# Kernel tuning notes

Measured on AMD Instinct MI355X. Metric: run time of the kernel, lower is better.

The kernel has to match this reference:

```python
import jax, jax.numpy as jnp
import numpy as np

B, N, K = 8, 4096, 20          # 8 point clouds, 4096 points each, k=20 neighbors
C_IN, C_OUT = 64, 128
LN_EPS = 1e-5


def _layernorm(h, g, b):
    mu = jnp.mean(h, axis=-1, keepdims=True)
    var = jnp.var(h, axis=-1, keepdims=True)
    return (h - mu) * jax.lax.rsqrt(var + LN_EPS) * g + b


def setup_inputs() -> dict:
    key = jax.random.key(0)
    ks = jax.random.split(key, 8)
    x = jax.random.normal(ks[0], (B * N, C_IN), dtype=jnp.float32)
    batch = jnp.repeat(jnp.arange(B, dtype=jnp.int64), N)  # equal-size graphs
    def lin(k, fan_in, fan_out):
        bound = 1.0 / np.sqrt(fan_in)
        kw, kb = jax.random.split(k)
        W = jax.random.uniform(kw, (fan_in, fan_out), jnp.float32, -bound, bound)
        b = jax.random.uniform(kb, (fan_out,), jnp.float32, -bound, bound)
        return W, b
    W1, b1 = lin(ks[1], 2 * C_IN, C_OUT)
    W2, b2 = lin(ks[2], C_OUT, C_OUT)
    Wres, bres = lin(ks[3], C_IN, C_OUT)
    g1 = jnp.ones((C_OUT,), jnp.float32); be1 = jnp.zeros((C_OUT,), jnp.float32)
    g2 = jnp.ones((C_OUT,), jnp.float32); be2 = jnp.zeros((C_OUT,), jnp.float32)
    return dict(x=x, batch=batch, W1=W1, b1=b1, g1=g1, be1=be1,
                W2=W2, b2=b2, g2=g2, be2=be2, Wres=Wres, bres=bres)


def reference(x, batch, W1, b1, g1, be1, W2, b2, g2, be2, Wres, bres):
    # batch is contiguous equal-size segments -> reshape to [B, N, C]
    xb = x.reshape(B, N, C_IN)
    # KNN in feature space per cloud (DynamicEdgeConv semantics)
    sq = jnp.sum(xb * xb, axis=-1)                                 # [B, N]
    d2 = sq[:, :, None] + sq[:, None, :] - 2.0 * jnp.einsum('bnc,bmc->bnm', xb, xb)
    _, idx = jax.lax.top_k(-d2, K)                                  # [B, N, K], includes self
    # gather neighbor features
    xj = jnp.take_along_axis(xb[:, None, :, :].repeat(1, axis=1),
                             idx[..., None], axis=2) if False else \
         jax.vmap(lambda pts, ids: pts[ids])(xb, idx)               # [B, N, K, C_IN]
    xi = jnp.broadcast_to(xb[:, :, None, :], xj.shape)
    e = jnp.concatenate([xi, xj - xi], axis=-1)                     # [B, N, K, 2*C_IN]
    h = jax.nn.relu(_layernorm(jnp.einsum('bnkc,cd->bnkd', e, W1) + b1, g1, be1))
    h = jax.nn.relu(_layernorm(jnp.einsum('bnkd,de->bnke', h, W2) + b2, g2, be2))
    agg = jnp.max(h, axis=2)                                        # max aggregation over k
    out = agg.reshape(B * N, C_OUT) + (x @ Wres + bres)             # residual projection
    return out
```

## Files before the change

kernel.cpp:

```cpp
#include <hip/hip_runtime.h>
#include <hip/hip_bf16.h>


#define NB 8
#define NPTS 4096
#define KNN 20
#define NTOT (NB * NPTS)
#define NEDGE (NTOT * KNN)
#define LDA 136

typedef short bf16x8 __attribute__((ext_vector_type(8)));
typedef float f32x4 __attribute__((ext_vector_type(4)));

__device__ __forceinline__ unsigned short f2bf(float f) {
    union { float f; unsigned u; } v; v.f = f;
    unsigned r = v.u + 0x7FFFu + ((v.u >> 16) & 1u);
    return (unsigned short)(r >> 16);
}
__device__ __forceinline__ float bf2f(unsigned short s) {
    union { unsigned u; float f; } v; v.u = ((unsigned)s) << 16;
    return v.f;
}

__global__ __launch_bounds__(256) void k_prep(const float* __restrict__ x,
                                              unsigned short* __restrict__ xhi,
                                              unsigned short* __restrict__ xlo,
                                              float* __restrict__ sqn) {
    int id = blockIdx.x * 2048 + threadIdx.x * 8;
    float4 v0 = *(const float4*)(x + id);
    float4 v1 = *(const float4*)(x + id + 4);
    float vs[8] = {v0.x, v0.y, v0.z, v0.w, v1.x, v1.y, v1.z, v1.w};
    unsigned short h[8], l[8];
    float s = 0.f;
#pragma unroll
    for (int i = 0; i < 8; ++i) {
        h[i] = f2bf(vs[i]);
        l[i] = f2bf(vs[i] - bf2f(h[i]));
        s += vs[i] * vs[i];
    }
    uint4 hp, lp;
    hp.x = h[0] | ((unsigned)h[1] << 16); hp.y = h[2] | ((unsigned)h[3] << 16);
    hp.z = h[4] | ((unsigned)h[5] << 16); hp.w = h[6] | ((unsigned)h[7] << 16);
    lp.x = l[0] | ((unsigned)l[1] << 16); lp.y = l[2] | ((unsigned)l[3] << 16);
    lp.z = l[4] | ((unsigned)l[5] << 16); lp.w = l[6] | ((unsigned)l[7] << 16);
    *(uint4*)(xhi + id) = hp;
    *(uint4*)(xlo + id) = lp;
    s += __shfl_xor(s, 1); s += __shfl_xor(s, 2); s += __shfl_xor(s, 4);
    if ((threadIdx.x & 7) == 0) sqn[id >> 6] = -0.5f * s;
}

__global__ __launch_bounds__(256) void k_wt(const float* __restrict__ W1, const float* __restrict__ W2,
                                            const float* __restrict__ Wres,
                                            unsigned short* __restrict__ wa, unsigned short* __restrict__ wb,
                                            unsigned short* __restrict__ wrt, unsigned short* __restrict__ w2p) {
    int id = blockIdx.x * 256 + threadIdx.x;
    if (id < 16384) {
        int f = id >> 9, pos = id & 511;
        int lane = pos >> 3, m = pos & 7;
        int ks = f >> 3, nt = f & 7;
        int lr = lane & 15, kg = lane >> 4;
        int c = ks * 32 + kg * 8 + m;
        int d = nt * 16 + lr;
        w2p[id] = f2bf(W2[c * 128 + d]);
    } else if (id < 24576) {
        int i = id - 16384;
        int d = i >> 6, c = i & 63;
        wa[i] = f2bf(W1[c * 128 + d] - W1[(64 + c) * 128 + d]);
    } else if (id < 32768) {
        int i = id - 24576;
        int d = i >> 6, c = i & 63;
        wb[i] = f2bf(W1[(64 + c) * 128 + d]);
    } else {
        int i = id - 32768;
        int d = i >> 6, c = i & 63;
        wrt[i] = f2bf(Wres[c * 128 + d]);
    }
}

__global__ __launch_bounds__(512, 4) void k_knn(const float* __restrict__ x,
                                                const unsigned short* __restrict__ xhi,
                                                const unsigned short* __restrict__ xlo,
                                                const float* __restrict__ sqn,
                                                int* __restrict__ knn_idx) {
    int b  = blockIdx.x & 7;
    int qb = blockIdx.x >> 3;
    int t  = threadIdx.x;
    int w = t >> 6, lane = t & 63;
    int lr = lane & 15, kg = lane >> 4;
    int qgrp = w >> 1, tp = w & 1;
    int n0  = b * NPTS + qb * 64;
    int cb0 = b * NPTS;

    __shared__ union {
        unsigned short ring[2][2][8][512];
        struct { float md[64][161]; int ci[64][24]; } m;
        struct { float ce[64][24]; } r;
    } U;

    int qg = n0 + qgrp * 16 + lr;
    bf16x8 qhi0 = *(const bf16x8*)(xhi + (size_t)qg * 64 + kg * 8);
    bf16x8 qhi1 = *(const bf16x8*)(xhi + (size_t)qg * 64 + 32 + kg * 8);
    bf16x8 qlo0 = *(const bf16x8*)(xlo + (size_t)qg * 64 + kg * 8);
    bf16x8 qlo1 = *(const bf16x8*)(xlo + (size_t)qg * 64 + 32 + kg * 8);

    const unsigned short* splane = ((w >> 1) & 1) ? xlo : xhi;
    int stt = w >> 2, skh = w & 1;
    size_t soff = (size_t)(stt * 16 + (lane & 15)) * 64 + skh * 32 + (lane >> 4) * 8;

    float kd[KNN];
#pragma unroll
    for (int p = 0; p < KNN; ++p) kd[p] = 3.4e38f;
    int myq = qgrp * 16 + lr;

    {
        uint4 p0 = *(const uint4*)(splane + (size_t)cb0 * 64 + soff);
        uint4 p1 = *(const uint4*)(splane + (size_t)(cb0 + 32) * 64 + soff);
        *(uint4*)&U.ring[0][0][w][lane * 8] = p0;
        *(uint4*)&U.ring[0][1][w][lane * 8] = p1;
    }
    uint4 g0 = *(const uint4*)(splane + (size_t)(cb0 + 64) * 64 + soff);
    uint4 g1 = *(const uint4*)(splane + (size_t)(cb0 + 96) * 64 + soff);
    float4 sqc0 = *(const float4*)&sqn[cb0 + tp * 32 + kg * 4];
    float4 sqc1 = *(const float4*)&sqn[cb0 + tp * 32 + 16 + kg * 4];
    __syncthreads();

#pragma unroll 1
    for (int s = 0; s < 64; ++s) {
        if (s + 1 < 64) {
            *(uint4*)&U.ring[(s + 1) & 1][0][w][lane * 8] = g0;
            *(uint4*)&U.ring[(s + 1) & 1][1][w][lane * 8] = g1;
        }
        if (s + 2 < 64) {
            g0 = *(const uint4*)(splane + (size_t)(cb0 + (2 * s + 4) * 32) * 64 + soff);
            g1 = *(const uint4*)(splane + (size_t)(cb0 + (2 * s + 5) * 32) * 64 + soff);
        }
        float4 nsq0, nsq1;
        if (s + 1 < 64) {
            nsq0 = *(const float4*)&sqn[cb0 + (2 * (s + 1) + tp) * 32 + kg * 4];
            nsq1 = *(const float4*)&sqn[cb0 + (2 * (s + 1) + tp) * 32 + 16 + kg * 4];
        }

        const unsigned short* fr = &U.ring[s & 1][tp][0][0];
        bf16x8 A0 = *(const bf16x8*)(fr + 0 * 512 + lane * 8);
        bf16x8 A1 = *(const bf16x8*)(fr + 1 * 512 + lane * 8);
        bf16x8 A2 = *(const bf16x8*)(fr + 2 * 512 + lane * 8);
        bf16x8 A3 = *(const bf16x8*)(fr + 3 * 512 + lane * 8);
        bf16x8 A4 = *(const bf16x8*)(fr + 4 * 512 + lane * 8);
        bf16x8 A5 = *(const bf16x8*)(fr + 5 * 512 + lane * 8);
        bf16x8 A6 = *(const bf16x8*)(fr + 6 * 512 + lane * 8);
        bf16x8 A7 = *(const bf16x8*)(fr + 7 * 512 + lane * 8);

        f32x4 a00 = {sqc0.x, sqc0.y, sqc0.z, sqc0.w};
        f32x4 a01 = {0.f, 0.f, 0.f, 0.f};
        f32x4 a10 = {sqc1.x, sqc1.y, sqc1.z, sqc1.w};
        f32x4 a11 = {0.f, 0.f, 0.f, 0.f};
        a00 = __builtin_amdgcn_mfma_f32_16x16x32_bf16(A0, qhi0, a00, 0, 0, 0);
        a10 = __builtin_amdgcn_mfma_f32_16x16x32_bf16(A4, qhi0, a10, 0, 0, 0);
        a01 = __builtin_amdgcn_mfma_f32_16x16x32_bf16(A1, qhi1, a01, 0, 0, 0);
        a11 = __builtin_amdgcn_mfma_f32_16x16x32_bf16(A5, qhi1, a11, 0, 0, 0);
        a00 = __builtin_amdgcn_mfma_f32_16x16x32_bf16(A2, qhi0, a00, 0, 0, 0);
        a10 = __builtin_amdgcn_mfma_f32_16x16x32_bf16(A6, qhi0, a10, 0, 0, 0);
        a01 = __builtin_amdgcn_mfma_f32_16x16x32_bf16(A3, qhi1, a01, 0, 0, 0);
        a11 = __builtin_amdgcn_mfma_f32_16x16x32_bf16(A7, qhi1, a11, 0, 0, 0);
        a00 = __builtin_amdgcn_mfma_f32_16x16x32_bf16(A0, qlo0, a00, 0, 0, 0);
        a10 = __builtin_amdgcn_mfma_f32_16x16x32_bf16(A4, qlo0, a10, 0, 0, 0);
        a01 = __builtin_amdgcn_mfma_f32_16x16x32_bf16(A1, qlo1, a01, 0, 0, 0);
        a11 = __builtin_amdgcn_mfma_f32_16x16x32_bf16(A5, qlo1, a11, 0, 0, 0);

        int ibase = (2 * s + tp) * 32 + kg * 4;
#pragma unroll
        for (int j = 0; j < 8; ++j) {
            float sc = (j < 4) ? -(a00[j & 3] + a01[j & 3]) : -(a10[j & 3] + a11[j & 3]);
            unsigned idx12 = (unsigned)(ibase + ((j >> 2) << 4) + (j & 3));
            float xv = __uint_as_float((__float_as_uint(sc) & 0xFFFFF000u) | idx12);
#pragma unroll
            for (int p = KNN - 1; p >= 1; --p)
                kd[p] = __builtin_amdgcn_fmed3f(xv, kd[p - 1], kd[p]);
            kd[0] = fminf(kd[0], xv);
        }

        __syncthreads();
        sqc0 = nsq0; sqc1 = nsq1;
    }

    __syncthreads();
#pragma unroll
    for (int p = 0; p < KNN; ++p) U.m.md[myq][(tp * 4 + kg) * KNN + p] = kd[p];
    __syncthreads();

    if (t < 64) {
        float kdm[24];
#pragma unroll
        for (int s2 = 0; s2 < 24; ++s2) kdm[s2] = 3.4e38f;
        float km = 3.4e38f;
#pragma unroll 1
        for (int u = 0; u < 8; ++u) {
#pragma unroll 1
            for (int p = 0; p < KNN; ++p) {
                float d = U.m.md[t][u * KNN + p];
                if (d >= km) break;
#pragma unroll
                for (int s2 = 23; s2 >= 1; --s2)
                    kdm[s2] = __builtin_amdgcn_fmed3f(d, kdm[s2 - 1], kdm[s2]);
                kdm[0] = fminf(kdm[0], d);
                km = kdm[23];
            }
        }
#pragma unroll
        for (int s2 = 0; s2 < 24; ++s2)
            U.m.ci[t][s2] = (int)(__float_as_uint(kdm[s2]) & 0xFFFu) + cb0;
    }
    __syncthreads();

#pragma unroll 1
    for (int task = t; task < 1536; task += 512) {
        int q = task / 24, sl = task - q * 24;
        int cidx = U.m.ci[q][sl];
        const float* xqp = x + (size_t)(n0 + q) * 64;
        const float* xc  = x + (size_t)cidx * 64;
        float dot = 0.f;
#pragma unroll
        for (int g = 0; g < 16; ++g) {
            float4 a = *(const float4*)(xqp + g * 4);
            float4 bb = *(const float4*)(xc + g * 4);
            dot += a.x * bb.x + a.y * bb.y + a.z * bb.z + a.w * bb.w;
        }
        U.r.ce[q][sl] = -sqn[cidx] - dot;
    }
    __syncthreads();

    if (t < 64) {
        float ev[24]; int iv[24];
#pragma unroll
        for (int s2 = 0; s2 < 24; ++s2) { ev[s2] = U.r.ce[t][s2]; iv[s2] = U.m.ci[t][s2]; }
        unsigned mask = 0;
#pragma unroll
        for (int pass = 0; pass < 4; ++pass) {
            float best = -3.4e38f; int bid = -1, bs = 0;
#pragma unroll
            for (int s2 = 0; s2 < 24; ++s2) {
                bool free_ = ((mask >> s2) & 1u) == 0u;
                bool gt = (ev[s2] > best) || (ev[s2] == best && iv[s2] > bid);
                if (free_ && gt) { best = ev[s2]; bid = iv[s2]; bs = s2; }
            }
            mask |= 1u << bs;
        }
        int* op = knn_idx + (size_t)(n0 + t) * KNN;
        int pos = 0;
#pragma unroll
        for (int s2 = 0; s2 < 24; ++s2)
            if (((mask >> s2) & 1u) == 0u) op[pos++] = iv[s2];
    }
}

__global__ __launch_bounds__(256) void k_ybres(const unsigned short* __restrict__ xhi,
                                               const unsigned short* __restrict__ wb,
                                               const unsigned short* __restrict__ wrt,
                                               const float* __restrict__ bres,
                                               unsigned short* __restrict__ Yb,
                                               float* __restrict__ out) {
    int t = threadIdx.x;
    int wv = t >> 6, lane = t & 63;
    int lr = lane & 15, kg = lane >> 4;
    int n0 = blockIdx.x * 64 + wv * 16;

    bf16x8 af0 = *(const bf16x8*)(xhi + (size_t)(n0 + lr) * 64 + kg * 8);
    bf16x8 af1 = *(const bf16x8*)(xhi + (size_t)(n0 + lr) * 64 + 32 + kg * 8);

    f32x4 accY[8], accR[8];
#pragma unroll
    for (int nt = 0; nt < 8; ++nt) {
        accY[nt] = (f32x4){0.f, 0.f, 0.f, 0.f};
        float bv = bres[nt * 16 + lr];
        accR[nt] = (f32x4){bv, bv, bv, bv};
    }
#pragma unroll
    for (int nt = 0; nt < 8; ++nt) {
        bf16x8 b0 = *(const bf16x8*)(wb + (size_t)(nt * 16 + lr) * 64 + kg * 8);
        bf16x8 b1 = *(const bf16x8*)(wb + (size_t)(nt * 16 + lr) * 64 + 32 + kg * 8);
        accY[nt] = __builtin_amdgcn_mfma_f32_16x16x32_bf16(af0, b0, accY[nt], 0, 0, 0);
        accY[nt] = __builtin_amdgcn_mfma_f32_16x16x32_bf16(af1, b1, accY[nt], 0, 0, 0);
        bf16x8 r0 = *(const bf16x8*)(wrt + (size_t)(nt * 16 + lr) * 64 + kg * 8);
        bf16x8 r1 = *(const bf16x8*)(wrt + (size_t)(nt * 16 + lr) * 64 + 32 + kg * 8);
        accR[nt] = __builtin_amdgcn_mfma_f32_16x16x32_bf16(af0, r0, accR[nt], 0, 0, 0);
        accR[nt] = __builtin_amdgcn_mfma_f32_16x16x32_bf16(af1, r1, accR[nt], 0, 0, 0);
    }
#pragma unroll
    for (int nt = 0; nt < 8; ++nt)
#pragma unroll
        for (int j = 0; j < 4; ++j) {
            Yb[(size_t)(n0 + kg * 4 + j) * 128 + nt * 16 + lr] = f2bf(accY[nt][j]);
            out[(size_t)(n0 + kg * 4 + j) * 128 + nt * 16 + lr] = accR[nt][j];
        }
}

__device__ __forceinline__ void ln_relu_store(f32x4 acc[2][8], unsigned short* A, int wv, int lane,
                                              const float* __restrict__ bias, const float* __restrict__ g,
                                              const float* __restrict__ be) {
    int lc = lane & 15, kg = lane >> 4;
    float bv[8], gv[8], bev[8];
#pragma unroll
    for (int nt = 0; nt < 8; ++nt) {
        bv[nt]  = bias[nt * 16 + lc];
        gv[nt]  = g[nt * 16 + lc];
        bev[nt] = be[nt * 16 + lc];
    }
#pragma unroll
    for (int mt = 0; mt < 2; ++mt) {
#pragma unroll
        for (int j = 0; j < 4; ++j) {
            float v[8]; float s = 0.f, ss = 0.f;
#pragma unroll
            for (int nt = 0; nt < 8; ++nt) {
                v[nt] = acc[mt][nt][j] + bv[nt];
                s += v[nt]; ss += v[nt] * v[nt];
            }
#pragma unroll
            for (int m = 1; m < 16; m <<= 1) { s += __shfl_xor(s, m); ss += __shfl_xor(ss, m); }
            float mean = s * 0.0078125f;
            float var  = ss * 0.0078125f - mean * mean;
            float rstd = rsqrtf(fmaxf(var, 0.f) + 1e-5f);
            int row = wv * 32 + mt * 16 + kg * 4 + j;
#pragma unroll
            for (int nt = 0; nt < 8; ++nt) {
                float h = (v[nt] - mean) * rstd * gv[nt] + bev[nt];
                h = fmaxf(h, 0.f);
                A[(size_t)row * LDA + nt * 16 + lc] = f2bf(h);
            }
        }
    }
}

__global__ __launch_bounds__(320, 2) void k_edge(const float* __restrict__ x, const int* __restrict__ knn_idx,
                                                 const unsigned short* __restrict__ Yb,
                                                 const unsigned short* __restrict__ w2p,
                                                 const unsigned short* __restrict__ wa,
                                                 const float* __restrict__ b1, const float* __restrict__ g1, const float* __restrict__ be1,
                                                 const float* __restrict__ b2, const float* __restrict__ g2, const float* __restrict__ be2,
                                                 float* __restrict__ out) {
    __shared__ unsigned short A[160 * LDA];
    __shared__ unsigned short W2s[32 * 512];
    __shared__ float Ya8[8][128];
    __shared__ float GB[256];
    int t = threadIdx.x;
    int bid = blockIdx.x;
    int blk = (bid & 7) * 512 + (bid >> 3);

    for (int id = t; id < 2048; id += 320)
        *(uint4*)&W2s[id * 8] = *(const uint4*)(w2p + (size_t)id * 8);
    if (t < 32)       *(float4*)&GB[t * 4] = *(const float4*)(g1 + t * 4);
    else if (t < 64)  *(float4*)&GB[t * 4] = *(const float4*)(be1 + (t - 32) * 4);

    int r = t >> 1, h = t & 1;
    int eg = blk * 160 + r;
    int ploc = r / 20;
    int jn = knn_idx[eg];
    uint4 ybr[8];
    {
        const unsigned short* ybp = Yb + (size_t)jn * 128 + h * 64;
#pragma unroll
        for (int i = 0; i < 8; ++i) ybr[i] = *(const uint4*)(ybp + i * 8);
    }

    if (t < 64) {
        int lane = t, lr = lane & 15, kg = lane >> 4;
        int prow = blk * 8 + (lr & 7);
        const float* xp = x + (size_t)prow * 64;
        bf16x8 af0, af1;
        {
            union { unsigned short u[8]; bf16x8 v; } cv;
            float4 u0 = *(const float4*)(xp + kg * 8);
            float4 u1 = *(const float4*)(xp + kg * 8 + 4);
            cv.u[0] = f2bf(u0.x); cv.u[1] = f2bf(u0.y); cv.u[2] = f2bf(u0.z); cv.u[3] = f2bf(u0.w);
            cv.u[4] = f2bf(u1.x); cv.u[5] = f2bf(u1.y); cv.u[6] = f2bf(u1.z); cv.u[7] = f2bf(u1.w);
            af0 = cv.v;
            float4 w0 = *(const float4*)(xp + 32 + kg * 8);
            float4 w1 = *(const float4*)(xp + 32 + kg * 8 + 4);
            cv.u[0] = f2bf(w0.x); cv.u[1] = f2bf(w0.y); cv.u[2] = f2bf(w0.z); cv.u[3] = f2bf(w0.w);
            cv.u[4] = f2bf(w1.x); cv.u[5] = f2bf(w1.y); cv.u[6] = f2bf(w1.z); cv.u[7] = f2bf(w1.w);
            af1 = cv.v;
        }
        f32x4 accA[8];
#pragma unroll
        for (int nt = 0; nt < 8; ++nt) {
            float bv = b1[nt * 16 + lr];
            accA[nt] = (f32x4){bv, bv, bv, bv};
        }
#pragma unroll
        for (int nt = 0; nt < 8; ++nt) {
            bf16x8 b0 = *(const bf16x8*)(wa + (size_t)(nt * 16 + lr) * 64 + kg * 8);
            bf16x8 b1f = *(const bf16x8*)(wa + (size_t)(nt * 16 + lr) * 64 + 32 + kg * 8);
            accA[nt] = __builtin_amdgcn_mfma_f32_16x16x32_bf16(af0, b0, accA[nt], 0, 0, 0);
            accA[nt] = __builtin_amdgcn_mfma_f32_16x16x32_bf16(af1, b1f, accA[nt], 0, 0, 0);
        }
#pragma unroll
        for (int nt = 0; nt < 8; ++nt)
#pragma unroll
            for (int j = 0; j < 4; ++j) {
                int rr = kg * 4 + j;
                if (rr < 8) Ya8[rr][nt * 16 + lr] = accA[nt][j];
            }
    }
    __syncthreads();

    {
        float v[64]; float s = 0.f, ss = 0.f;
#pragma unroll
        for (int i = 0; i < 8; ++i) {
            unsigned uu[4] = {ybr[i].x, ybr[i].y, ybr[i].z, ybr[i].w};
#pragma unroll
            for (int k2 = 0; k2 < 4; ++k2) {
                int c = h * 64 + i * 8 + 2 * k2;
                float w0 = Ya8[ploc][c]     + bf2f((unsigned short)(uu[k2] & 0xFFFFu));
                float w1 = Ya8[ploc][c + 1] + bf2f((unsigned short)(uu[k2] >> 16));
                v[i * 8 + 2 * k2] = w0; v[i * 8 + 2 * k2 + 1] = w1;
                s += w0 + w1; ss += w0 * w0 + w1 * w1;
            }
        }
        s += __shfl_xor(s, 1); ss += __shfl_xor(ss, 1);
        float mean = s * 0.0078125f;
        float var  = ss * 0.0078125f - mean * mean;
        float rstd = rsqrtf(fmaxf(var, 0.f) + 1e-5f);
#pragma unroll
        for (int i = 0; i < 8; ++i) {
            unsigned short hh[8];
#pragma unroll
            for (int k2 = 0; k2 < 8; ++k2) {
                int c = h * 64 + i * 8 + k2;
                float hv = (v[i * 8 + k2] - mean) * rstd * GB[c] + GB[128 + c];
                hh[k2] = f2bf(fmaxf(hv, 0.f));
            }
            uint4 pk;
            pk.x = hh[0] | ((unsigned)hh[1] << 16); pk.y = hh[2] | ((unsigned)hh[3] << 16);
            pk.z = hh[4] | ((unsigned)hh[5] << 16); pk.w = hh[6] | ((unsigned)hh[7] << 16);
            *(uint4*)&A[(size_t)r * LDA + h * 64 + i * 8] = pk;
        }
    }

    int wv = t >> 6, lane = t & 63;
    int lr = lane & 15, kg = lane >> 4;
    f32x4 acc2[2][8];
#pragma unroll
    for (int i = 0; i < 2; ++i)
#pragma unroll
        for (int j = 0; j < 8; ++j) acc2[i][j] = (f32x4){0.f, 0.f, 0.f, 0.f};
#pragma unroll
    for (int ks = 0; ks < 4; ++ks) {
        int ko = ks * 32 + kg * 8;
        bf16x8 a0 = *(const bf16x8*)(A + (size_t)(wv * 32 + lr) * LDA + ko);
        bf16x8 a1 = *(const bf16x8*)(A + (size_t)(wv * 32 + 16 + lr) * LDA + ko);
#pragma unroll
        for (int nt = 0; nt < 8; ++nt) {
            bf16x8 bf = *(const bf16x8*)&W2s[(size_t)(ks * 8 + nt) * 512 + lane * 8];
            acc2[0][nt] = __builtin_amdgcn_mfma_f32_16x16x32_bf16(a0, bf, acc2[0][nt], 0, 0, 0);
            acc2[1][nt] = __builtin_amdgcn_mfma_f32_16x16x32_bf16(a1, bf, acc2[1][nt], 0, 0, 0);
        }
    }
    ln_relu_store(acc2, A, wv, lane, b2, g2, be2);

    __syncthreads();

    if (t < 128) {
        int p = t >> 4, cg = t & 15;
        int n = blk * 8 + p;
        float mx[8];
#pragma unroll
        for (int k = 0; k < 8; ++k) mx[k] = 0.f;
#pragma unroll
        for (int rr = 0; rr < 20; ++rr) {
            uint4 vv = *(const uint4*)&A[(size_t)(p * 20 + rr) * LDA + cg * 8];
            unsigned uu[4] = {vv.x, vv.y, vv.z, vv.w};
#pragma unroll
            for (int k = 0; k < 4; ++k) {
                float lo = __uint_as_float(uu[k] << 16);
                float hi = __uint_as_float(uu[k] & 0xFFFF0000u);
                mx[2 * k]     = fmaxf(mx[2 * k], lo);
                mx[2 * k + 1] = fmaxf(mx[2 * k + 1], hi);
            }
        }
        float* op = out + (size_t)n * 128 + cg * 8;
        float4 o0 = *(float4*)op;
        float4 o1 = *(float4*)(op + 4);
        o0.x += mx[0]; o0.y += mx[1]; o0.z += mx[2]; o0.w += mx[3];
        o1.x += mx[4]; o1.y += mx[5]; o1.z += mx[6]; o1.w += mx[7];
        *(float4*)op = o0;
        *(float4*)(op + 4) = o1;
    }
}

extern "C" void kernel_launch(void* const* d_in, const int* in_sizes, int n_in,
                              void* d_out, int out_size, void* d_ws, size_t ws_size,
                              hipStream_t stream) {
    const float* x    = (const float*)d_in[0];
    const float* W1   = (const float*)d_in[2];
    const float* b1   = (const float*)d_in[3];
    const float* g1   = (const float*)d_in[4];
    const float* be1  = (const float*)d_in[5];
    const float* W2   = (const float*)d_in[6];
    const float* b2   = (const float*)d_in[7];
    const float* g2   = (const float*)d_in[8];
    const float* be2  = (const float*)d_in[9];
    const float* Wres = (const float*)d_in[10];
    const float* bres = (const float*)d_in[11];
    float* out = (float*)d_out;

    char* ws = (char*)d_ws;
    float* sqn           = (float*)(ws);
    unsigned short* wa   = (unsigned short*)(ws + 131072);
    unsigned short* wb   = (unsigned short*)(ws + 147456);
    unsigned short* wrt  = (unsigned short*)(ws + 163840);
    unsigned short* w2p  = (unsigned short*)(ws + 180224);
    int* knn_idx         = (int*)(ws + 212992);
    unsigned short* Yb   = (unsigned short*)(ws + 2834432);

    unsigned short* xhi = (unsigned short*)d_out;
    unsigned short* xlo = (unsigned short*)((char*)d_out + 4194304);

    k_prep  <<<dim3(1024),      dim3(256), 0, stream>>>(x, xhi, xlo, sqn);
    k_wt    <<<dim3(160),       dim3(256), 0, stream>>>(W1, W2, Wres, wa, wb, wrt, w2p);
    k_knn   <<<dim3(NB * 64),   dim3(512), 0, stream>>>(x, xhi, xlo, sqn, knn_idx);
    k_ybres <<<dim3(NTOT / 64), dim3(256), 0, stream>>>(xhi, wb, wrt, bres, Yb, out);
    k_edge  <<<dim3(NEDGE / 160), dim3(320), 0, stream>>>(x, knn_idx, Yb, w2p, wa,
                                                          b1, g1, be1, b2, g2, be2, out);
}
```

Baseline: 383.4 us.

## Halve KNN query tile and split candidates four ways per block

The KNN kernel now handles 32 queries per block instead of 64, with four waves per query group each scanning a quarter of the candidate tiles. The grid doubles to 1024 blocks. Only the hi bf16 plane of candidates is staged to shared memory, and squared norms are loaded directly each step. The merge of per-lane top-k lists runs in two phases over a 28-entry refinement buffer instead of 24. The aim is more parallelism and less per-block work and shared memory, at the cost of more merge work per query and more redundant candidate streaming across blocks.

```diff
diff --git a/kernel.cpp b/kernel.cpp
--- a/kernel.cpp
+++ b/kernel.cpp
@@ -8,6 +8,7 @@
 #define NTOT (NB * NPTS)
 #define NEDGE (NTOT * KNN)
 #define LDA 136
+#define RB 28
 
 typedef short bf16x8 __attribute__((ext_vector_type(8)));
 typedef float f32x4 __attribute__((ext_vector_type(4)));
@@ -87,15 +88,16 @@
     int t  = threadIdx.x;
     int w = t >> 6, lane = t & 63;
     int lr = lane & 15, kg = lane >> 4;
-    int qgrp = w >> 1, tp = w & 1;
-    int n0  = b * NPTS + qb * 64;
+    int qgrp = w >> 2, tp = w & 3;
+    int n0  = b * NPTS + qb * 32;
     int cb0 = b * NPTS;
 
     __shared__ union {
-        unsigned short ring[2][2][8][512];
-        struct { float md[64][161]; int ci[64][24]; } m;
-        struct { float ce[64][24]; } r;
+        unsigned short ring[2][4][4][512];
+        struct { float md[32][161]; } m;
+        struct { float ce[32][29]; } r;
     } U;
+    __shared__ int ci[32][29];
 
     int qg = n0 + qgrp * 16 + lr;
     bf16x8 qhi0 = *(const bf16x8*)(xhi + (size_t)qg * 64 + kg * 8);
@@ -103,9 +105,7 @@
     bf16x8 qlo0 = *(const bf16x8*)(xlo + (size_t)qg * 64 + kg * 8);
     bf16x8 qlo1 = *(const bf16x8*)(xlo + (size_t)qg * 64 + 32 + kg * 8);
 
-    const unsigned short* splane = ((w >> 1) & 1) ? xlo : xhi;
-    int stt = w >> 2, skh = w & 1;
-    size_t soff = (size_t)(stt * 16 + (lane & 15)) * 64 + skh * 32 + (lane >> 4) * 8;
+    size_t soff = (size_t)(qgrp * 16 + lr) * 64 + kg * 8;
 
     float kd[KNN];
 #pragma unroll
@@ -113,61 +113,54 @@
     int myq = qgrp * 16 + lr;
 
     {
-        uint4 p0 = *(const uint4*)(splane + (size_t)cb0 * 64 + soff);
-        uint4 p1 = *(const uint4*)(splane + (size_t)(cb0 + 32) * 64 + soff);
-        *(uint4*)&U.ring[0][0][w][lane * 8] = p0;
-        *(uint4*)&U.ring[0][1][w][lane * 8] = p1;
-    }
-    uint4 g0 = *(const uint4*)(splane + (size_t)(cb0 + 64) * 64 + soff);
-    uint4 g1 = *(const uint4*)(splane + (size_t)(cb0 + 96) * 64 + soff);
-    float4 sqc0 = *(const float4*)&sqn[cb0 + tp * 32 + kg * 4];
-    float4 sqc1 = *(const float4*)&sqn[cb0 + tp * 32 + 16 + kg * 4];
+        const unsigned short* sp = xhi + (size_t)(cb0 + tp * 32) * 64 + soff;
+        uint4 p0 = *(const uint4*)sp;
+        uint4 p1 = *(const uint4*)(sp + 32);
+        *(uint4*)&U.ring[0][tp][2 * qgrp][lane * 8] = p0;
+        *(uint4*)&U.ring[0][tp][2 * qgrp + 1][lane * 8] = p1;
+    }
+    uint4 g0, g1;
+    {
+        const unsigned short* sp = xhi + (size_t)(cb0 + (4 + tp) * 32) * 64 + soff;
+        g0 = *(const uint4*)sp;
+        g1 = *(const uint4*)(sp + 32);
+    }
     __syncthreads();
 
 #pragma unroll 1
-    for (int s = 0; s < 64; ++s) {
-        if (s + 1 < 64) {
-            *(uint4*)&U.ring[(s + 1) & 1][0][w][lane * 8] = g0;
-            *(uint4*)&U.ring[(s + 1) & 1][1][w][lane * 8] = g1;
-        }
-        if (s + 2 < 64) {
-            g0 = *(const uint4*)(splane + (size_t)(cb0 + (2 * s + 4) * 32) * 64 + soff);
-            g1 = *(const uint4*)(splane + (size_t)(cb0 + (2 * s + 5) * 32) * 64 + soff);
-        }
-        float4 nsq0, nsq1;
-        if (s + 1 < 64) {
-            nsq0 = *(const float4*)&sqn[cb0 + (2 * (s + 1) + tp) * 32 + kg * 4];
-            nsq1 = *(const float4*)&sqn[cb0 + (2 * (s + 1) + tp) * 32 + 16 + kg * 4];
-        }
+    for (int s = 0; s < 32; ++s) {
+        int cbT = cb0 + (4 * s + tp) * 32;
+        if (s + 1 < 32) {
+            *(uint4*)&U.ring[(s + 1) & 1][tp][2 * qgrp][lane * 8] = g0;
+            *(uint4*)&U.ring[(s + 1) & 1][tp][2 * qgrp + 1][lane * 8] = g1;
+        }
+        if (s + 2 < 32) {
+            const unsigned short* sp = xhi + (size_t)(cb0 + (4 * (s + 2) + tp) * 32) * 64 + soff;
+            g0 = *(const uint4*)sp;
+            g1 = *(const uint4*)(sp + 32);
+        }
+
+        f32x4 a00 = *(const f32x4*)&sqn[cbT + kg * 4];
+        f32x4 a10 = *(const f32x4*)&sqn[cbT + 16 + kg * 4];
+        f32x4 a01 = {0.f, 0.f, 0.f, 0.f};
+        f32x4 a11 = {0.f, 0.f, 0.f, 0.f};
 
         const unsigned short* fr = &U.ring[s & 1][tp][0][0];
         bf16x8 A0 = *(const bf16x8*)(fr + 0 * 512 + lane * 8);
         bf16x8 A1 = *(const bf16x8*)(fr + 1 * 512 + lane * 8);
         bf16x8 A2 = *(const bf16x8*)(fr + 2 * 512 + lane * 8);
         bf16x8 A3 = *(const bf16x8*)(fr + 3 * 512 + lane * 8);
-        bf16x8 A4 = *(const bf16x8*)(fr + 4 * 512 + lane * 8);
-        bf16x8 A5 = *(const bf16x8*)(fr + 5 * 512 + lane * 8);
-        bf16x8 A6 = *(const bf16x8*)(fr + 6 * 512 + lane * 8);
-        bf16x8 A7 = *(const bf16x8*)(fr + 7 * 512 + lane * 8);
-
-        f32x4 a00 = {sqc0.x, sqc0.y, sqc0.z, sqc0.w};
-        f32x4 a01 = {0.f, 0.f, 0.f, 0.f};
-        f32x4 a10 = {sqc1.x, sqc1.y, sqc1.z, sqc1.w};
-        f32x4 a11 = {0.f, 0.f, 0.f, 0.f};
+
         a00 = __builtin_amdgcn_mfma_f32_16x16x32_bf16(A0, qhi0, a00, 0, 0, 0);
-        a10 = __builtin_amdgcn_mfma_f32_16x16x32_bf16(A4, qhi0, a10, 0, 0, 0);
+        a10 = __builtin_amdgcn_mfma_f32_16x16x32_bf16(A2, qhi0, a10, 0, 0, 0);
         a01 = __builtin_amdgcn_mfma_f32_16x16x32_bf16(A1, qhi1, a01, 0, 0, 0);
-        a11 = __builtin_amdgcn_mfma_f32_16x16x32_bf16(A5, qhi1, a11, 0, 0, 0);
-        a00 = __builtin_amdgcn_mfma_f32_16x16x32_bf16(A2, qhi0, a00, 0, 0, 0);
-        a10 = __builtin_amdgcn_mfma_f32_16x16x32_bf16(A6, qhi0, a10, 0, 0, 0);
-        a01 = __builtin_amdgcn_mfma_f32_16x16x32_bf16(A3, qhi1, a01, 0, 0, 0);
-        a11 = __builtin_amdgcn_mfma_f32_16x16x32_bf16(A7, qhi1, a11, 0, 0, 0);
+        a11 = __builtin_amdgcn_mfma_f32_16x16x32_bf16(A3, qhi1, a11, 0, 0, 0);
         a00 = __builtin_amdgcn_mfma_f32_16x16x32_bf16(A0, qlo0, a00, 0, 0, 0);
-        a10 = __builtin_amdgcn_mfma_f32_16x16x32_bf16(A4, qlo0, a10, 0, 0, 0);
+        a10 = __builtin_amdgcn_mfma_f32_16x16x32_bf16(A2, qlo0, a10, 0, 0, 0);
         a01 = __builtin_amdgcn_mfma_f32_16x16x32_bf16(A1, qlo1, a01, 0, 0, 0);
-        a11 = __builtin_amdgcn_mfma_f32_16x16x32_bf16(A5, qlo1, a11, 0, 0, 0);
-
-        int ibase = (2 * s + tp) * 32 + kg * 4;
+        a11 = __builtin_amdgcn_mfma_f32_16x16x32_bf16(A3, qlo1, a11, 0, 0, 0);
+
+        int ibase = (4 * s + tp) * 32 + kg * 4;
 #pragma unroll
         for (int j = 0; j < 8; ++j) {
             float sc = (j < 4) ? -(a00[j & 3] + a01[j & 3]) : -(a10[j & 3] + a11[j & 3]);
@@ -180,19 +173,20 @@
         }
 
         __syncthreads();
-        sqc0 = nsq0; sqc1 = nsq1;
-    }
-
-    __syncthreads();
-#pragma unroll
-    for (int p = 0; p < KNN; ++p) U.m.md[myq][(tp * 4 + kg) * KNN + p] = kd[p];
-    __syncthreads();
-
-    if (t < 64) {
-        float kdm[24];
-#pragma unroll
-        for (int s2 = 0; s2 < 24; ++s2) kdm[s2] = 3.4e38f;
-        float km = 3.4e38f;
+    }
+
+    float kdm[RB];
+    float km = 3.4e38f;
+
+    if (tp < 2) {
+#pragma unroll
+        for (int p = 0; p < KNN; ++p)
+            U.m.md[myq][(tp * 4 + kg) * KNN + p] = kd[p];
+    }
+    __syncthreads();
+    if (t < 32) {
+#pragma unroll
+        for (int s2 = 0; s2 < RB; ++s2) kdm[s2] = 3.4e38f;
 #pragma unroll 1
         for (int u = 0; u < 8; ++u) {
 #pragma unroll 1
@@ -200,22 +194,44 @@
                 float d = U.m.md[t][u * KNN + p];
                 if (d >= km) break;
 #pragma unroll
-                for (int s2 = 23; s2 >= 1; --s2)
+                for (int s2 = RB - 1; s2 >= 1; --s2)
                     kdm[s2] = __builtin_amdgcn_fmed3f(d, kdm[s2 - 1], kdm[s2]);
                 kdm[0] = fminf(kdm[0], d);
-                km = kdm[23];
-            }
-        }
-#pragma unroll
-        for (int s2 = 0; s2 < 24; ++s2)
-            U.m.ci[t][s2] = (int)(__float_as_uint(kdm[s2]) & 0xFFFu) + cb0;
-    }
-    __syncthreads();
-
+                km = kdm[RB - 1];
+            }
+        }
+    }
+    __syncthreads();
+    if (tp >= 2) {
+#pragma unroll
+        for (int p = 0; p < KNN; ++p)
+            U.m.md[myq][((tp - 2) * 4 + kg) * KNN + p] = kd[p];
+    }
+    __syncthreads();
+    if (t < 32) {
 #pragma unroll 1
-    for (int task = t; task < 1536; task += 512) {
-        int q = task / 24, sl = task - q * 24;
-        int cidx = U.m.ci[q][sl];
+        for (int u = 0; u < 8; ++u) {
+#pragma unroll 1
+            for (int p = 0; p < KNN; ++p) {
+                float d = U.m.md[t][u * KNN + p];
+                if (d >= km) break;
+#pragma unroll
+                for (int s2 = RB - 1; s2 >= 1; --s2)
+                    kdm[s2] = __builtin_amdgcn_fmed3f(d, kdm[s2 - 1], kdm[s2]);
+                kdm[0] = fminf(kdm[0], d);
+                km = kdm[RB - 1];
+            }
+        }
+#pragma unroll
+        for (int s2 = 0; s2 < RB; ++s2)
+            ci[t][s2] = (int)(__float_as_uint(kdm[s2]) & 0xFFFu) + cb0;
+    }
+    __syncthreads();
+
+#pragma unroll 1
+    for (int task = t; task < 32 * RB; task += 512) {
+        int q = task / RB, sl = task - q * RB;
+        int cidx = ci[q][sl];
         const float* xqp = x + (size_t)(n0 + q) * 64;
         const float* xc  = x + (size_t)cidx * 64;
         float dot = 0.f;
@@ -229,16 +245,16 @@
     }
     __syncthreads();
 
-    if (t < 64) {
-        float ev[24]; int iv[24];
-#pragma unroll
-        for (int s2 = 0; s2 < 24; ++s2) { ev[s2] = U.r.ce[t][s2]; iv[s2] = U.m.ci[t][s2]; }
+    if (t < 32) {
+        float ev[RB]; int iv[RB];
+#pragma unroll
+        for (int s2 = 0; s2 < RB; ++s2) { ev[s2] = U.r.ce[t][s2]; iv[s2] = ci[t][s2]; }
         unsigned mask = 0;
 #pragma unroll
-        for (int pass = 0; pass < 4; ++pass) {
+        for (int pass = 0; pass < RB - KNN; ++pass) {
             float best = -3.4e38f; int bid = -1, bs = 0;
 #pragma unroll
-            for (int s2 = 0; s2 < 24; ++s2) {
+            for (int s2 = 0; s2 < RB; ++s2) {
                 bool free_ = ((mask >> s2) & 1u) == 0u;
                 bool gt = (ev[s2] > best) || (ev[s2] == best && iv[s2] > bid);
                 if (free_ && gt) { best = ev[s2]; bid = iv[s2]; bs = s2; }
@@ -248,7 +264,7 @@
         int* op = knn_idx + (size_t)(n0 + t) * KNN;
         int pos = 0;
 #pragma unroll
-        for (int s2 = 0; s2 < 24; ++s2)
+        for (int s2 = 0; s2 < RB; ++s2)
             if (((mask >> s2) & 1u) == 0u) op[pos++] = iv[s2];
     }
 }
@@ -518,7 +534,7 @@
 
     k_prep  <<<dim3(1024),      dim3(256), 0, stream>>>(x, xhi, xlo, sqn);
     k_wt    <<<dim3(160),       dim3(256), 0, stream>>>(W1, W2, Wres, wa, wb, wrt, w2p);
-    k_knn   <<<dim3(NB * 64),   dim3(512), 0, stream>>>(x, xhi, xlo, sqn, knn_idx);
+    k_knn   <<<dim3(NB * 128),  dim3(512), 0, stream>>>(x, xhi, xlo, sqn, knn_idx);
     k_ybres <<<dim3(NTOT / 64), dim3(256), 0, stream>>>(xhi, wb, wrt, bres, Yb, out);
     k_edge  <<<dim3(NEDGE / 160), dim3(320), 0, stream>>>(x, knn_idx, Yb, w2p, wa,
                                                           b1, g1, be1, b2, g2, be2, out);
```

Result: slower. 425.4 us (+11.0%).
